# Optimization experiments

Measured on AMD Instinct MI355X. Metric: run time of the kernel, lower is better.

## Reference

```python
import jax, jax.numpy as jnp
import numpy as np

N_EMBD = 1024
N_HEAD = 16
HEAD_DIM = N_EMBD // N_HEAD
NEG = -1e10


def setup_inputs() -> dict:
    key = jax.random.key(0)
    ks = jax.random.split(key, 5)
    B, T, C = 4, 2048, N_EMBD
    s = 0.02
    return {
        "x": jax.random.normal(ks[0], (B, T, C), dtype=jnp.float32),
        "w_attn": jax.random.normal(ks[1], (C, 3 * C), dtype=jnp.float32) * s,
        "b_attn": jnp.zeros((3 * C,), dtype=jnp.float32),
        "w_proj": jax.random.normal(ks[2], (C, C), dtype=jnp.float32) * s,
        "b_proj": jnp.zeros((C,), dtype=jnp.float32),
    }


def reference(x, w_attn, b_attn, w_proj, b_proj):
    B, T, C = x.shape
    H, D = N_HEAD, HEAD_DIM
    qkv = x @ w_attn + b_attn                      # [B,T,3C]
    q, k, v = jnp.split(qkv, 3, axis=-1)
    q = q.reshape(B, T, H, D).transpose(0, 2, 1, 3)  # [B,H,T,D]
    k = k.reshape(B, T, H, D).transpose(0, 2, 1, 3)
    v = v.reshape(B, T, H, D).transpose(0, 2, 1, 3)
    att = jnp.einsum("bhqd,bhkd->bhqk", q, k) / jnp.sqrt(jnp.float32(D))
    # additive causal mask: strictly-upper triangle gets -1e10 (as in torch source)
    mask = jnp.triu(jnp.full((T, T), NEG, dtype=att.dtype), k=1)
    att = jax.nn.softmax(att + mask, axis=-1)
    y = jnp.einsum("bhqk,bhkd->bhqd", att, v)      # [B,H,T,D]
    y = y.transpose(0, 2, 1, 3).reshape(B, T, C)
    return y @ w_proj + b_proj
```

## Files before the change

kernel.cpp:

```cpp
#include <hip/hip_runtime.h>
#include <hip/hip_bf16.h>

#define T_SEQ 2048
#define NE    1024
#define NH    16
#define HD    64
#define QKV_N 3072
#define MROWS 8192

typedef __attribute__((ext_vector_type(8))) short short8;
typedef __attribute__((ext_vector_type(4))) float f32x4;

__device__ __forceinline__ short f2bf(float f) {
  __hip_bfloat16 h = __float2bfloat16(f);
  return *reinterpret_cast<short*>(&h);
}

__device__ __forceinline__ void lds16(const void* g, void* l) {
  __builtin_amdgcn_global_load_lds(
      (const __attribute__((address_space(1))) unsigned int*)g,
      (__attribute__((address_space(3))) unsigned int*)l, 16, 0, 0);
}

__global__ __launch_bounds__(256) void prep_fused(const float* __restrict__ x,
                                                  short* __restrict__ xb,
                                                  const float* __restrict__ w_attn,
                                                  short* __restrict__ wT1) {
  __shared__ short tile[32][33];
  const int bid = blockIdx.x;
  if (bid < 4096) {
    const int i = bid * 256 + threadIdx.x;
    const float4* s = (const float4*)(x + (size_t)i * 8);
    float4 a = s[0], b = s[1];
    short8 v = short8{f2bf(a.x), f2bf(a.y), f2bf(a.z), f2bf(a.w),
                      f2bf(b.x), f2bf(b.y), f2bf(b.z), f2bf(b.w)};
    *(short8*)(xb + (size_t)i * 8) = v;
  } else {
    const int tb = bid - 4096;
    const int bn = (tb % 96) * 32;
    const int bk = (tb / 96) * 32;
    const int tx = threadIdx.x & 31;
    const int ty = threadIdx.x >> 5;
#pragma unroll
    for (int i = 0; i < 32; i += 8)
      tile[ty + i][tx] = f2bf(w_attn[(size_t)(bk + ty + i) * QKV_N + bn + tx]);
    __syncthreads();
#pragma unroll
    for (int i = 0; i < 32; i += 8)
      wT1[(size_t)(bn + ty + i) * NE + bk + tx] = tile[tx][ty + i];
  }
}

__global__ __launch_bounds__(256) void transpose_cvt(const float* __restrict__ src,
                                                     short* __restrict__ dst,
                                                     int K, int N) {
  __shared__ short tile[32][33];
  int bn = blockIdx.x * 32;
  int bk = blockIdx.y * 32;
  int tx = threadIdx.x;
  int ty = threadIdx.y;
#pragma unroll
  for (int i = 0; i < 32; i += 8)
    tile[ty + i][tx] = f2bf(src[(size_t)(bk + ty + i) * N + bn + tx]);
  __syncthreads();
#pragma unroll
  for (int i = 0; i < 32; i += 8)
    dst[(size_t)(bn + ty + i) * K + bk + tx] = tile[tx][ty + i];
}

template <bool OUTF32>
__global__ __launch_bounds__(256) void gemm_bt_bias(const short* __restrict__ A,
                                                    const short* __restrict__ Bt,
                                                    const float* __restrict__ bias,
                                                    void* __restrict__ Co,
                                                    int M, int N, int K) {
  __shared__ __align__(16) short As[128 * 64];
  __shared__ __align__(16) short Bs[128 * 64];

  const int m0 = blockIdx.x * 128;
  const int n0 = blockIdx.y * 128;
  const int tid = threadIdx.x;
  const int w = tid >> 6, lane = tid & 63;
  const int L15 = lane & 15, quad = lane >> 4;
  const int wr = (w >> 1) * 64, wc = (w & 1) * 64;

  const int srow = lane >> 3;
  const int sg = lane & 7;

  f32x4 acc[4][4] = {};

  for (int k0 = 0; k0 < K; k0 += 64) {
    __syncthreads();

#pragma unroll
    for (int p = 0; p < 4; ++p) {
      int r = p * 32 + w * 8 + srow;
      int gl = sg ^ (r & 7);
      lds16(A + (size_t)(m0 + r) * K + k0 + gl * 8, (char*)As + p * 4096 + w * 1024);
      lds16(Bt + (size_t)(n0 + r) * K + k0 + gl * 8, (char*)Bs + p * 4096 + w * 1024);
    }

    __syncthreads();

#pragma unroll
    for (int kk = 0; kk < 2; ++kk) {
      short8 af[4], bfr[4];
#pragma unroll
      for (int i = 0; i < 4; ++i) {
        int r = wr + i * 16 + L15;
        af[i] = *(const short8*)(As + r * 64 + (((kk * 4 + quad) ^ (r & 7)) * 8));
      }
#pragma unroll
      for (int j = 0; j < 4; ++j) {
        int r = wc + j * 16 + L15;
        bfr[j] = *(const short8*)(Bs + r * 64 + (((kk * 4 + quad) ^ (r & 7)) * 8));
      }
#pragma unroll
      for (int i = 0; i < 4; ++i)
#pragma unroll
        for (int j = 0; j < 4; ++j)
          acc[i][j] = __builtin_amdgcn_mfma_f32_16x16x32_bf16(af[i], bfr[j], acc[i][j], 0, 0, 0);
    }
  }

  float bv[4];
#pragma unroll
  for (int j = 0; j < 4; ++j) bv[j] = bias[n0 + wc + j * 16 + L15];
#pragma unroll
  for (int i = 0; i < 4; ++i)
#pragma unroll
    for (int j = 0; j < 4; ++j)
#pragma unroll
      for (int r = 0; r < 4; ++r) {
        size_t row = (size_t)(m0 + wr + i * 16 + quad * 4 + r);
        int col = n0 + wc + j * 16 + L15;
        float v = acc[i][j][r] + bv[j];
        if (OUTF32)
          ((float*)Co)[row * N + col] = v;
        else
          ((short*)Co)[row * N + col] = f2bf(v);
      }
}

__global__ __launch_bounds__(256) void attn_flash(const short* __restrict__ qkv,
                                                  short* __restrict__ y) {
  const int bx = blockIdx.x;
  const int bh = blockIdx.y;
  const int b = bh >> 4, h = bh & 15;
  const short* base = qkv + (size_t)b * T_SEQ * QKV_N;
  const int tid = threadIdx.x;
  const int w = tid >> 6, lane = tid & 63;
  const int L15 = lane & 15, quad = lane >> 4;

  __shared__ __align__(16) short Ks[64 * 80];
  __shared__ __align__(16) short Vts[64 * 80];
  __shared__ __align__(16) short Ps[4][32 * 72];

  const short one = (short)0x3F80;
  const short8 vone = short8{one, one, one, one, one, one, one, one};

  const float cs = 0.18033688011112042f;

  const short* kbase = base + NE + h * HD;
  const short* vbase = base + 2 * NE + h * HD;

  const int skey = tid >> 3;
  const int sd0 = (tid & 7) * 8;
  const int dv0 = w * 8;

#pragma unroll 1
  for (int seg = 0; seg < 2; ++seg) {
    const int qt = seg == 0 ? (T_SEQ / 128 - 1 - bx) : bx;

    short8 qf[2][2];
#pragma unroll
    for (int qs = 0; qs < 2; ++qs) {
      const short* qp =
          base + (size_t)(qt * 128 + w * 32 + qs * 16 + L15) * QKV_N + h * HD + quad * 8;
      qf[qs][0] = *(const short8*)qp;
      qf[qs][1] = *(const short8*)(qp + 32);
    }

    f32x4 O[2][4] = {};
    f32x4 L[2] = {};

    uint4 kv0 = *(const uint4*)(kbase + (size_t)skey * QKV_N + sd0);
    uint4 kv1 = *(const uint4*)(kbase + (size_t)(32 + skey) * QKV_N + sd0);
    uint4 vv0 = *(const uint4*)(vbase + (size_t)lane * QKV_N + dv0);
    uint4 vv1 = *(const uint4*)(vbase + (size_t)lane * QKV_N + dv0 + 32);

    const int nkt = 2 * qt + 2;
    for (int kt = 0; kt < nkt; ++kt) {
      __syncthreads();
      *(uint4*)&Ks[skey * 80 + sd0] = kv0;
      *(uint4*)&Ks[(32 + skey) * 80 + sd0] = kv1;
      {
        const short* pv0 = (const short*)&vv0;
        const short* pv1 = (const short*)&vv1;
#pragma unroll
        for (int j = 0; j < 8; ++j) {
          Vts[(dv0 + j) * 80 + lane] = pv0[j];
          Vts[(32 + dv0 + j) * 80 + lane] = pv1[j];
        }
      }
      __syncthreads();

      if (kt < nkt - 1) {
        int nt = kt + 1;
        kv0 = *(const uint4*)(kbase + (size_t)(nt * 64 + skey) * QKV_N + sd0);
        kv1 = *(const uint4*)(kbase + (size_t)(nt * 64 + 32 + skey) * QKV_N + sd0);
        vv0 = *(const uint4*)(vbase + (size_t)(nt * 64 + lane) * QKV_N + dv0);
        vv1 = *(const uint4*)(vbase + (size_t)(nt * 64 + lane) * QKV_N + dv0 + 32);
      }

      f32x4 S[2][4] = {};
#pragma unroll
      for (int nb = 0; nb < 4; ++nb) {
        short8 kb0 = *(const short8*)&Ks[(nb * 16 + L15) * 80 + quad * 8];
        short8 kb1 = *(const short8*)&Ks[(nb * 16 + L15) * 80 + 32 + quad * 8];
#pragma unroll
        for (int qs = 0; qs < 2; ++qs) {
          S[qs][nb] = __builtin_amdgcn_mfma_f32_16x16x32_bf16(qf[qs][0], kb0, S[qs][nb], 0, 0, 0);
          S[qs][nb] = __builtin_amdgcn_mfma_f32_16x16x32_bf16(qf[qs][1], kb1, S[qs][nb], 0, 0, 0);
        }
      }

      if (kt >= nkt - 2) {
#pragma unroll
        for (int qs = 0; qs < 2; ++qs)
#pragma unroll
          for (int nb = 0; nb < 4; ++nb) {
            int kg = kt * 64 + nb * 16 + L15;
#pragma unroll
            for (int r = 0; r < 4; ++r) {
              int qg = qt * 128 + w * 32 + qs * 16 + quad * 4 + r;
              if (kg > qg) S[qs][nb][r] = -1e30f;
            }
          }
      }

      short* myP = &Ps[w][0];
#pragma unroll
      for (int qs = 0; qs < 2; ++qs)
#pragma unroll
        for (int nb = 0; nb < 4; ++nb)
#pragma unroll
          for (int r = 0; r < 4; ++r)
            myP[(qs * 16 + quad * 4 + r) * 72 + nb * 16 + L15] =
                f2bf(__builtin_amdgcn_exp2f(S[qs][nb][r] * cs));
      asm volatile("" ::: "memory");
      short8 pf[2][2];
#pragma unroll
      for (int qs = 0; qs < 2; ++qs) {
        pf[qs][0] = *(const short8*)&myP[(qs * 16 + L15) * 72 + quad * 8];
        pf[qs][1] = *(const short8*)&myP[(qs * 16 + L15) * 72 + 32 + quad * 8];
      }

#pragma unroll
      for (int nb = 0; nb < 4; ++nb) {
        short8 vf0 = *(const short8*)&Vts[(nb * 16 + L15) * 80 + quad * 8];
        short8 vf1 = *(const short8*)&Vts[(nb * 16 + L15) * 80 + 32 + quad * 8];
#pragma unroll
        for (int qs = 0; qs < 2; ++qs) {
          O[qs][nb] = __builtin_amdgcn_mfma_f32_16x16x32_bf16(pf[qs][0], vf0, O[qs][nb], 0, 0, 0);
          O[qs][nb] = __builtin_amdgcn_mfma_f32_16x16x32_bf16(pf[qs][1], vf1, O[qs][nb], 0, 0, 0);
        }
      }
#pragma unroll
      for (int qs = 0; qs < 2; ++qs) {
        L[qs] = __builtin_amdgcn_mfma_f32_16x16x32_bf16(pf[qs][0], vone, L[qs], 0, 0, 0);
        L[qs] = __builtin_amdgcn_mfma_f32_16x16x32_bf16(pf[qs][1], vone, L[qs], 0, 0, 0);
      }
    }

#pragma unroll
    for (int qs = 0; qs < 2; ++qs) {
      float inv[4];
#pragma unroll
      for (int r = 0; r < 4; ++r) inv[r] = 1.0f / L[qs][r];
#pragma unroll
      for (int nb = 0; nb < 4; ++nb)
#pragma unroll
        for (int r = 0; r < 4; ++r) {
          size_t row =
              (size_t)b * T_SEQ + (size_t)(qt * 128 + w * 32 + qs * 16 + quad * 4 + r);
          int col = h * HD + nb * 16 + L15;
          y[row * NE + col] = f2bf(O[qs][nb][r] * inv[r]);
        }
    }
  }
}

extern "C" void kernel_launch(void* const* d_in, const int* in_sizes, int n_in,
                              void* d_out, int out_size, void* d_ws, size_t ws_size,
                              hipStream_t stream) {
  (void)in_sizes; (void)n_in; (void)out_size; (void)ws_size;
  const float* x      = (const float*)d_in[0];
  const float* w_attn = (const float*)d_in[1];
  const float* b_attn = (const float*)d_in[2];
  const float* w_proj = (const float*)d_in[3];
  const float* b_proj = (const float*)d_in[4];
  float* out = (float*)d_out;

  short* qkv = (short*)d_ws;
  short* wT2 = qkv;
  short* wT1 = qkv + (size_t)MROWS * QKV_N;
  short* y   = wT1;

  short* xb = (short*)d_out;

  prep_fused<<<4096 + 3072, 256, 0, stream>>>(x, xb, w_attn, wT1);

  gemm_bt_bias<false><<<dim3(MROWS / 128, QKV_N / 128), 256, 0, stream>>>(
      xb, wT1, b_attn, qkv, MROWS, QKV_N, NE);

  attn_flash<<<dim3(8, 64), 256, 0, stream>>>(qkv, y);

  transpose_cvt<<<dim3(NE / 32, NE / 32), dim3(32, 8), 0, stream>>>(w_proj, wT2, NE, NE);

  gemm_bt_bias<true><<<dim3(MROWS / 128, NE / 128), 256, 0, stream>>>(
      y, wT2, b_proj, out, MROWS, NE, NE);
}
```

Baseline: 257.8 us.

## Use two waves with 64 query rows each in flash attention

Reworks the attention kernel from four waves of 32 query rows into two waves of 64 query rows each, so every wave reuses each K/V tile loaded from LDS for twice as many rows. The staging loads are redistributed so 128 threads still fill the 64x64 K and transposed V tiles. This cuts LDS fragment reads per MFMA and barrier participants, at the cost of doubling per-thread registers (S, O, qf) and halving threads per block, which may reduce occupancy and latency hiding.

```diff
diff --git a/kernel.cpp b/kernel.cpp
--- a/kernel.cpp
+++ b/kernel.cpp
@@ -142,8 +142,8 @@
       }
 }
 
-__global__ __launch_bounds__(256) void attn_flash(const short* __restrict__ qkv,
-                                                  short* __restrict__ y) {
+__global__ __launch_bounds__(128, 2) void attn_flash(const short* __restrict__ qkv,
+                                                     short* __restrict__ y) {
   const int bx = blockIdx.x;
   const int bh = blockIdx.y;
   const int b = bh >> 4, h = bh & 15;
@@ -154,7 +154,7 @@
 
   __shared__ __align__(16) short Ks[64 * 80];
   __shared__ __align__(16) short Vts[64 * 80];
-  __shared__ __align__(16) short Ps[4][32 * 72];
+  __shared__ __align__(16) short Ps[2][64 * 72];
 
   const short one = (short)0x3F80;
   const short8 vone = short8{one, one, one, one, one, one, one, one};
@@ -166,60 +166,74 @@
 
   const int skey = tid >> 3;
   const int sd0 = (tid & 7) * 8;
-  const int dv0 = w * 8;
+  const int dv0 = w * 16;
 
 #pragma unroll 1
   for (int seg = 0; seg < 2; ++seg) {
     const int qt = seg == 0 ? (T_SEQ / 128 - 1 - bx) : bx;
 
-    short8 qf[2][2];
-#pragma unroll
-    for (int qs = 0; qs < 2; ++qs) {
+    short8 qf[4][2];
+#pragma unroll
+    for (int qs = 0; qs < 4; ++qs) {
       const short* qp =
-          base + (size_t)(qt * 128 + w * 32 + qs * 16 + L15) * QKV_N + h * HD + quad * 8;
+          base + (size_t)(qt * 128 + w * 64 + qs * 16 + L15) * QKV_N + h * HD + quad * 8;
       qf[qs][0] = *(const short8*)qp;
       qf[qs][1] = *(const short8*)(qp + 32);
     }
 
-    f32x4 O[2][4] = {};
-    f32x4 L[2] = {};
-
-    uint4 kv0 = *(const uint4*)(kbase + (size_t)skey * QKV_N + sd0);
-    uint4 kv1 = *(const uint4*)(kbase + (size_t)(32 + skey) * QKV_N + sd0);
-    uint4 vv0 = *(const uint4*)(vbase + (size_t)lane * QKV_N + dv0);
-    uint4 vv1 = *(const uint4*)(vbase + (size_t)lane * QKV_N + dv0 + 32);
+    f32x4 O[4][4] = {};
+    f32x4 L[4] = {};
+
+    uint4 kv0 = *(const uint4*)(kbase + (size_t)(0 * 16 + skey) * QKV_N + sd0);
+    uint4 kv1 = *(const uint4*)(kbase + (size_t)(1 * 16 + skey) * QKV_N + sd0);
+    uint4 kv2 = *(const uint4*)(kbase + (size_t)(2 * 16 + skey) * QKV_N + sd0);
+    uint4 kv3 = *(const uint4*)(kbase + (size_t)(3 * 16 + skey) * QKV_N + sd0);
+    uint4 vv0  = *(const uint4*)(vbase + (size_t)lane * QKV_N + dv0);
+    uint4 vv0b = *(const uint4*)(vbase + (size_t)lane * QKV_N + dv0 + 8);
+    uint4 vv1  = *(const uint4*)(vbase + (size_t)lane * QKV_N + dv0 + 32);
+    uint4 vv1b = *(const uint4*)(vbase + (size_t)lane * QKV_N + dv0 + 40);
 
     const int nkt = 2 * qt + 2;
     for (int kt = 0; kt < nkt; ++kt) {
       __syncthreads();
-      *(uint4*)&Ks[skey * 80 + sd0] = kv0;
-      *(uint4*)&Ks[(32 + skey) * 80 + sd0] = kv1;
+      *(uint4*)&Ks[(0 * 16 + skey) * 80 + sd0] = kv0;
+      *(uint4*)&Ks[(1 * 16 + skey) * 80 + sd0] = kv1;
+      *(uint4*)&Ks[(2 * 16 + skey) * 80 + sd0] = kv2;
+      *(uint4*)&Ks[(3 * 16 + skey) * 80 + sd0] = kv3;
       {
-        const short* pv0 = (const short*)&vv0;
-        const short* pv1 = (const short*)&vv1;
+        const short* p0 = (const short*)&vv0;
+        const short* p0b = (const short*)&vv0b;
+        const short* p1 = (const short*)&vv1;
+        const short* p1b = (const short*)&vv1b;
 #pragma unroll
         for (int j = 0; j < 8; ++j) {
-          Vts[(dv0 + j) * 80 + lane] = pv0[j];
-          Vts[(32 + dv0 + j) * 80 + lane] = pv1[j];
+          Vts[(dv0 + j) * 80 + lane] = p0[j];
+          Vts[(dv0 + 8 + j) * 80 + lane] = p0b[j];
+          Vts[(32 + dv0 + j) * 80 + lane] = p1[j];
+          Vts[(40 + dv0 + j) * 80 + lane] = p1b[j];
         }
       }
       __syncthreads();
 
       if (kt < nkt - 1) {
         int nt = kt + 1;
-        kv0 = *(const uint4*)(kbase + (size_t)(nt * 64 + skey) * QKV_N + sd0);
-        kv1 = *(const uint4*)(kbase + (size_t)(nt * 64 + 32 + skey) * QKV_N + sd0);
-        vv0 = *(const uint4*)(vbase + (size_t)(nt * 64 + lane) * QKV_N + dv0);
-        vv1 = *(const uint4*)(vbase + (size_t)(nt * 64 + lane) * QKV_N + dv0 + 32);
-      }
-
-      f32x4 S[2][4] = {};
+        kv0 = *(const uint4*)(kbase + (size_t)(nt * 64 + 0 * 16 + skey) * QKV_N + sd0);
+        kv1 = *(const uint4*)(kbase + (size_t)(nt * 64 + 1 * 16 + skey) * QKV_N + sd0);
+        kv2 = *(const uint4*)(kbase + (size_t)(nt * 64 + 2 * 16 + skey) * QKV_N + sd0);
+        kv3 = *(const uint4*)(kbase + (size_t)(nt * 64 + 3 * 16 + skey) * QKV_N + sd0);
+        vv0  = *(const uint4*)(vbase + (size_t)(nt * 64 + lane) * QKV_N + dv0);
+        vv0b = *(const uint4*)(vbase + (size_t)(nt * 64 + lane) * QKV_N + dv0 + 8);
+        vv1  = *(const uint4*)(vbase + (size_t)(nt * 64 + lane) * QKV_N + dv0 + 32);
+        vv1b = *(const uint4*)(vbase + (size_t)(nt * 64 + lane) * QKV_N + dv0 + 40);
+      }
+
+      f32x4 S[4][4] = {};
 #pragma unroll
       for (int nb = 0; nb < 4; ++nb) {
         short8 kb0 = *(const short8*)&Ks[(nb * 16 + L15) * 80 + quad * 8];
         short8 kb1 = *(const short8*)&Ks[(nb * 16 + L15) * 80 + 32 + quad * 8];
 #pragma unroll
-        for (int qs = 0; qs < 2; ++qs) {
+        for (int qs = 0; qs < 4; ++qs) {
           S[qs][nb] = __builtin_amdgcn_mfma_f32_16x16x32_bf16(qf[qs][0], kb0, S[qs][nb], 0, 0, 0);
           S[qs][nb] = __builtin_amdgcn_mfma_f32_16x16x32_bf16(qf[qs][1], kb1, S[qs][nb], 0, 0, 0);
         }
@@ -227,13 +241,13 @@
 
       if (kt >= nkt - 2) {
 #pragma unroll
-        for (int qs = 0; qs < 2; ++qs)
+        for (int qs = 0; qs < 4; ++qs)
 #pragma unroll
           for (int nb = 0; nb < 4; ++nb) {
             int kg = kt * 64 + nb * 16 + L15;
 #pragma unroll
             for (int r = 0; r < 4; ++r) {
-              int qg = qt * 128 + w * 32 + qs * 16 + quad * 4 + r;
+              int qg = qt * 128 + w * 64 + qs * 16 + quad * 4 + r;
               if (kg > qg) S[qs][nb][r] = -1e30f;
             }
           }
@@ -241,7 +255,7 @@
 
       short* myP = &Ps[w][0];
 #pragma unroll
-      for (int qs = 0; qs < 2; ++qs)
+      for (int qs = 0; qs < 4; ++qs)
 #pragma unroll
         for (int nb = 0; nb < 4; ++nb)
 #pragma unroll
@@ -249,9 +263,9 @@
             myP[(qs * 16 + quad * 4 + r) * 72 + nb * 16 + L15] =
                 f2bf(__builtin_amdgcn_exp2f(S[qs][nb][r] * cs));
       asm volatile("" ::: "memory");
-      short8 pf[2][2];
-#pragma unroll
-      for (int qs = 0; qs < 2; ++qs) {
+      short8 pf[4][2];
+#pragma unroll
+      for (int qs = 0; qs < 4; ++qs) {
         pf[qs][0] = *(const short8*)&myP[(qs * 16 + L15) * 72 + quad * 8];
         pf[qs][1] = *(const short8*)&myP[(qs * 16 + L15) * 72 + 32 + quad * 8];
       }
@@ -261,20 +275,20 @@
         short8 vf0 = *(const short8*)&Vts[(nb * 16 + L15) * 80 + quad * 8];
         short8 vf1 = *(const short8*)&Vts[(nb * 16 + L15) * 80 + 32 + quad * 8];
 #pragma unroll
-        for (int qs = 0; qs < 2; ++qs) {
+        for (int qs = 0; qs < 4; ++qs) {
           O[qs][nb] = __builtin_amdgcn_mfma_f32_16x16x32_bf16(pf[qs][0], vf0, O[qs][nb], 0, 0, 0);
           O[qs][nb] = __builtin_amdgcn_mfma_f32_16x16x32_bf16(pf[qs][1], vf1, O[qs][nb], 0, 0, 0);
         }
       }
 #pragma unroll
-      for (int qs = 0; qs < 2; ++qs) {
+      for (int qs = 0; qs < 4; ++qs) {
         L[qs] = __builtin_amdgcn_mfma_f32_16x16x32_bf16(pf[qs][0], vone, L[qs], 0, 0, 0);
         L[qs] = __builtin_amdgcn_mfma_f32_16x16x32_bf16(pf[qs][1], vone, L[qs], 0, 0, 0);
       }
     }
 
 #pragma unroll
-    for (int qs = 0; qs < 2; ++qs) {
+    for (int qs = 0; qs < 4; ++qs) {
       float inv[4];
 #pragma unroll
       for (int r = 0; r < 4; ++r) inv[r] = 1.0f / L[qs][r];
@@ -283,7 +297,7 @@
 #pragma unroll
         for (int r = 0; r < 4; ++r) {
           size_t row =
-              (size_t)b * T_SEQ + (size_t)(qt * 128 + w * 32 + qs * 16 + quad * 4 + r);
+              (size_t)b * T_SEQ + (size_t)(qt * 128 + w * 64 + qs * 16 + quad * 4 + r);
           int col = h * HD + nb * 16 + L15;
           y[row * NE + col] = f2bf(O[qs][nb][r] * inv[r]);
         }
@@ -314,7 +328,7 @@
   gemm_bt_bias<false><<<dim3(MROWS / 128, QKV_N / 128), 256, 0, stream>>>(
       xb, wT1, b_attn, qkv, MROWS, QKV_N, NE);
 
-  attn_flash<<<dim3(8, 64), 256, 0, stream>>>(qkv, y);
+  attn_flash<<<dim3(8, 64), 128, 0, stream>>>(qkv, y);
 
   transpose_cvt<<<dim3(NE / 32, NE / 32), dim3(32, 8), 0, stream>>>(w_proj, wT2, NE, NE);
 
```

Result: slower. 296.6 us (+15.1%).
